# Optimization experiments

Hardware: AMD Instinct MI355X
Metric: run time of the kernel (lower is better)

Reference implementation:

```python
import jax, jax.numpy as jnp
import numpy as np

B, L, R, D = 64, 512, 512, 512
F_CONV, H = 100, 60

def setup_inputs() -> dict:
    key = jax.random.key(0)
    ks = jax.random.split(key, 8)
    l_lengths = jax.random.randint(ks[0], (B,), L // 2, L + 1)
    r_lengths = jax.random.randint(ks[1], (B,), R // 2, R + 1)
    l_vectors = jax.random.normal(ks[2], (L, B, D), jnp.float32)
    r_vectors = jax.random.normal(ks[3], (R, B, D), jnp.float32)
    Wconv = jax.random.normal(ks[4], (F_CONV, D), jnp.float32) / np.sqrt(D).astype(np.float32)
    bconv = jnp.zeros((F_CONV,), jnp.float32)
    Wd = jax.random.normal(ks[5], (H, 2 * F_CONV), jnp.float32) / np.sqrt(2 * F_CONV).astype(np.float32)
    bd = jnp.zeros((H,), jnp.float32)
    return {"l_lengths": l_lengths, "l_vectors": l_vectors, "r_lengths": r_lengths,
            "r_vectors": r_vectors, "Wconv": Wconv, "bconv": bconv, "Wd": Wd, "bd": bd}

def reference(l_lengths, l_vectors, r_lengths, r_vectors, Wconv, bconv, Wd, bd):
    Lm, Bm, Dm = l_vectors.shape
    Rm = r_vectors.shape[0]
    # masks, seq-first [L,B] like pad_sequence output
    l_mask = (jnp.arange(Lm)[:, None] < l_lengths[None, :]).astype(l_vectors.dtype)
    r_mask = (jnp.arange(Rm)[:, None] < r_lengths[None, :]).astype(r_vectors.dtype)
    lmT, rmT = l_mask.T, r_mask.T  # [B,L], [B,R]

    # co-attention scores [B,L,R]
    attention = jnp.einsum('lbd,rbd->blr', l_vectors, r_vectors)
    attention = attention * lmT[:, :, None] * rmT[:, None, :]

    att_r = jax.nn.softmax(attention - 10.0 * (1.0 - lmT[:, :, None]), axis=1)
    att_r = att_r * lmT[:, :, None]
    att_r = att_r / (att_r.sum(axis=1, keepdims=True) + 1e-13)

    att_l = jax.nn.softmax(attention - 10.0 * (1.0 - rmT[:, None, :]), axis=2)
    att_l = att_l * rmT[:, None, :]
    att_l = att_l / (att_l.sum(axis=2, keepdims=True) + 1e-13)

    # ---- left side: stats + top-1 hard attention ----
    rl = r_lengths.astype(l_vectors.dtype)[:, None]
    l_mean = att_l.sum(axis=2) / rl                              # [B,L]
    l_w = (att_l * att_l).sum(axis=2) / rl - l_mean * l_mean
    l_w = l_w / jnp.maximum(l_mean, 0.001)
    l_a = att_l.max(axis=2)                                      # top-1 value [B,L]
    l_i = att_l.argmax(axis=2)                                   # top-1 index [B,L]
    l_i = l_i * lmT.astype(l_i.dtype)
    l_a = l_a / jnp.maximum(l_a, 0.001)                          # k=1: sum == value
    gathered = jnp.take_along_axis(r_vectors, l_i.T[:, :, None], axis=0)  # [L,B,D]
    l_counter = l_a.T[:, :, None] * gathered
    l_c = l_w.T[:, :, None] * jnp.abs(l_vectors - l_counter) * l_mask[:, :, None]

    # ---- right side ----
    ll = l_lengths.astype(r_vectors.dtype)[:, None]
    r_mean = att_r.sum(axis=1) / ll                              # [B,R]
    r_w = (att_r * att_r).sum(axis=1) / ll - r_mean * r_mean
    r_w = r_w / jnp.maximum(r_mean, 0.001)
    r_a = att_r.max(axis=1)                                      # [B,R]
    r_i = att_r.argmax(axis=1)
    r_i = r_i * rmT.astype(r_i.dtype)
    r_a = r_a / jnp.maximum(r_a, 0.001)
    gathered_r = jnp.take_along_axis(l_vectors, r_i.T[:, :, None], axis=0)  # [R,B,D]
    r_counter = r_a.T[:, :, None] * gathered_r
    r_c = r_w.T[:, :, None] * jnp.abs(r_vectors - r_counter) * r_mask[:, :, None]

    # SentenceConv(1, 100, dim): kernel (1, dim) conv == per-position linear,
    # ReLU, masked max-pool over the sequence.
    def sconv(x, mask):  # x [S,B,D], mask [S,B]
        h = jax.nn.relu(jnp.einsum('sbd,fd->bsf', x, Wconv) + bconv)  # [B,S,F]
        h = h - (1.0 - mask.T)[:, :, None] * 1e9
        return h.max(axis=1)  # [B,F]

    feats = jnp.concatenate([sconv(l_c, l_mask), sconv(r_c, r_mask)], axis=1)  # [B,200]
    return jax.nn.relu(feats @ Wd.T + bd)  # [B,60]
```

## Files before the change

kernel.cpp:

```cpp
#include <hip/hip_runtime.h>
#include <math.h>

#define BB 64
#define LL 512
#define RR 512
#define DD 512
#define FC 100
#define FP 112
#define HH 60
#define BD (BB*DD)

typedef __attribute__((ext_vector_type(8))) short bf16x8;
typedef __attribute__((ext_vector_type(4))) float f32x4;

__device__ __forceinline__ unsigned short bf16rne(float x) {
  unsigned u = __float_as_uint(x);
  return (unsigned short)((u + 0x7fffu + ((u >> 16) & 1u)) >> 16);
}
__device__ __forceinline__ float bf16tof(unsigned short h) {
  return __uint_as_float((unsigned)h << 16);
}

__device__ __forceinline__ void split2(float x0, float x1, unsigned& h2, unsigned& l2) {
  unsigned u0 = __float_as_uint(x0), u1 = __float_as_uint(x1);
  h2 = __builtin_amdgcn_perm(u1, u0, 0x07060302u);
  float r0 = x0 - __uint_as_float(u0 & 0xffff0000u);
  float r1 = x1 - __uint_as_float(u1 & 0xffff0000u);
  l2 = __builtin_amdgcn_perm(__float_as_uint(r1), __float_as_uint(r0), 0x07060302u);
}

template <int N>
__device__ __forceinline__ float ror_max_f(float v) {
  return fmaxf(v, __uint_as_float(__builtin_amdgcn_mov_dpp(__float_as_uint(v), 0x120 | N, 0xf, 0xf, true)));
}
template <int N>
__device__ __forceinline__ float ror_add_f(float v) {
  return v + __uint_as_float(__builtin_amdgcn_mov_dpp(__float_as_uint(v), 0x120 | N, 0xf, 0xf, true));
}
template <int N>
__device__ __forceinline__ int ror_min_i(int v) {
  int o = __builtin_amdgcn_mov_dpp(v, 0x120 | N, 0xf, 0xf, true);
  return o < v ? o : v;
}
__device__ __forceinline__ float row16_max(float v) {
  v = ror_max_f<1>(v); v = ror_max_f<2>(v); v = ror_max_f<4>(v); return ror_max_f<8>(v);
}
__device__ __forceinline__ float row16_sum(float v) {
  v = ror_add_f<1>(v); v = ror_add_f<2>(v); v = ror_add_f<4>(v); return ror_add_f<8>(v);
}
__device__ __forceinline__ int row16_min(int v) {
  v = ror_min_i<1>(v); v = ror_min_i<2>(v); v = ror_min_i<4>(v); return ror_min_i<8>(v);
}

__global__ __launch_bounds__(512, 2) void gemm_att(const float* __restrict__ lv,
                                                   const float* __restrict__ rv,
                                                   const int* __restrict__ llen,
                                                   const int* __restrict__ rlen,
                                                   float4* __restrict__ lpart,
                                                   float4* __restrict__ rpart) {
  __shared__ __align__(16) unsigned short Ah[256][40];
  __shared__ __align__(16) unsigned short Al[256][40];
  __shared__ __align__(16) unsigned short Bh[256][40];
  __shared__ __align__(16) unsigned short Bl[256][40];

  const int bid = blockIdx.x;
  const int wid = (bid & 7) * 32 + (bid >> 3);
  const int b  = wid >> 2;
  const int l0 = ((wid >> 1) & 1) * 256;
  const int r0 = (wid & 1) * 256;

  const int t = threadIdx.x;
  const int srow = t >> 1;
  const int half = t & 1;
  const int kq = half * 16;

  const float* Abase = lv + (size_t)(l0 + srow) * BD + b * DD + kq;
  const float* Bbase = rv + (size_t)(r0 + srow) * BD + b * DD + kq;

  float4 pa[4], pb[4];
#pragma unroll
  for (int q = 0; q < 4; ++q) {
    pa[q] = *(const float4*)(Abase + q * 4);
    pb[q] = *(const float4*)(Bbase + q * 4);
  }

  const int lane = t & 63;
  const int wv = t >> 6;
  const int wrow = wv >> 2;
  const int wcol = wv & 3;
  const int fr = lane & 15;
  const int kh = lane >> 4;

  f32x4 acc[8][4];
#pragma unroll
  for (int i = 0; i < 8; ++i)
#pragma unroll
    for (int j = 0; j < 4; ++j) acc[i][j] = (f32x4){0.f, 0.f, 0.f, 0.f};

  for (int it = 0; it < 16; ++it) {
    __syncthreads();
#pragma unroll
    for (int q = 0; q < 4; ++q) {
      unsigned h01, l01, h23, l23;
      split2(pa[q].x, pa[q].y, h01, l01);
      split2(pa[q].z, pa[q].w, h23, l23);
      *(uint2*)&Ah[srow][kq + q * 4] = make_uint2(h01, h23);
      *(uint2*)&Al[srow][kq + q * 4] = make_uint2(l01, l23);
      split2(pb[q].x, pb[q].y, h01, l01);
      split2(pb[q].z, pb[q].w, h23, l23);
      *(uint2*)&Bh[srow][kq + q * 4] = make_uint2(h01, h23);
      *(uint2*)&Bl[srow][kq + q * 4] = make_uint2(l01, l23);
    }
    if (it < 15) {
      const float* An = Abase + (it + 1) * 32;
      const float* Bn = Bbase + (it + 1) * 32;
#pragma unroll
      for (int q = 0; q < 4; ++q) {
        pa[q] = *(const float4*)(An + q * 4);
        pb[q] = *(const float4*)(Bn + q * 4);
      }
    }
    __syncthreads();

    bf16x8 bh[4], bl[4];
#pragma unroll
    for (int j = 0; j < 4; ++j) {
      bh[j] = *(const bf16x8*)&Bh[wcol * 64 + j * 16 + fr][kh * 8];
      bl[j] = *(const bf16x8*)&Bl[wcol * 64 + j * 16 + fr][kh * 8];
    }
#pragma unroll
    for (int i = 0; i < 8; ++i) {
      bf16x8 ah = *(const bf16x8*)&Ah[wrow * 128 + i * 16 + fr][kh * 8];
      bf16x8 al = *(const bf16x8*)&Al[wrow * 128 + i * 16 + fr][kh * 8];
#pragma unroll
      for (int j = 0; j < 4; ++j) {
        acc[i][j] = __builtin_amdgcn_mfma_f32_16x16x32_bf16(ah, bh[j], acc[i][j], 0, 0, 0);
        acc[i][j] = __builtin_amdgcn_mfma_f32_16x16x32_bf16(ah, bl[j], acc[i][j], 0, 0, 0);
        acc[i][j] = __builtin_amdgcn_mfma_f32_16x16x32_bf16(al, bh[j], acc[i][j], 0, 0, 0);
      }
    }
  }

  const int ll_ = llen[b], rl_ = rlen[b];
  __syncthreads();
  float4* rowsc = (float4*)&Ah[0][0];
  float4* colsc = (float4*)&Bh[0][0];

  const int rbase = r0 + wcol * 64 + fr;
  bool vr4[4]; int rr4[4];
#pragma unroll
  for (int j = 0; j < 4; ++j) { rr4[j] = rbase + j * 16; vr4[j] = rr4[j] < rl_; }

#pragma unroll
  for (int i = 0; i < 8; ++i) {
#pragma unroll
    for (int q = 0; q < 4; ++q) {
      const int trow = wrow * 128 + i * 16 + kh * 4 + q;
      const bool vl = (l0 + trow) < ll_;
      float s[4];
      float M = -1e30f;
#pragma unroll
      for (int j = 0; j < 4; ++j) {
        float raw = acc[i][j][q];
        s[j] = !vr4[j] ? -10.f : (vl ? raw : 0.f);
        M = fmaxf(M, s[j]);
      }
      M = row16_max(M);
      float zv = 0.f, q2 = 0.f;
      int loc = 0x7fffffff;
#pragma unroll
      for (int j = 0; j < 4; ++j) {
        float e = __expf(s[j] - M);
        if (vr4[j]) {
          zv += e; q2 += e * e;
          if (s[j] == M && rr4[j] < loc) loc = rr4[j];
        }
      }
      zv = row16_sum(zv);
      q2 = row16_sum(q2);
      loc = row16_min(loc);
      if (fr == 0)
        rowsc[wcol * 256 + trow] = make_float4(M, zv, q2, __int_as_float(loc));
    }
  }

#pragma unroll
  for (int j = 0; j < 4; ++j) {
    const int tcol = wcol * 64 + j * 16 + fr;
    const bool vr = (r0 + tcol) < rl_;
    float M = -1e30f;
#pragma unroll
    for (int i = 0; i < 8; ++i)
#pragma unroll
      for (int q = 0; q < 4; ++q) {
        int lg = l0 + wrow * 128 + i * 16 + kh * 4 + q;
        bool vl = lg < ll_;
        float sv = !vl ? -10.f : (vr ? acc[i][j][q] : 0.f);
        M = fmaxf(M, sv);
      }
    M = fmaxf(M, __shfl_xor(M, 16, 64));
    M = fmaxf(M, __shfl_xor(M, 32, 64));
    float zv = 0.f, q2 = 0.f;
    int loc = 0x7fffffff;
#pragma unroll
    for (int i = 0; i < 8; ++i)
#pragma unroll
      for (int q = 0; q < 4; ++q) {
        int lg = l0 + wrow * 128 + i * 16 + kh * 4 + q;
        bool vl = lg < ll_;
        float sv = !vl ? -10.f : (vr ? acc[i][j][q] : 0.f);
        float e = __expf(sv - M);
        if (vl) {
          zv += e; q2 += e * e;
          if (sv == M && lg < loc) loc = lg;
        }
      }
    zv += __shfl_xor(zv, 16, 64); zv += __shfl_xor(zv, 32, 64);
    q2 += __shfl_xor(q2, 16, 64); q2 += __shfl_xor(q2, 32, 64);
    { int o = __shfl_xor(loc, 16, 64); loc = o < loc ? o : loc; }
    { int o = __shfl_xor(loc, 32, 64); loc = o < loc ? o : loc; }
    if (kh == 0)
      colsc[wrow * 256 + tcol] = make_float4(M, zv, q2, __int_as_float(loc));
  }

  __syncthreads();

  if (t < 256) {
    float4 p = rowsc[t];
    float M = p.x, zv = p.y, q2 = p.z;
    int loc = __float_as_int(p.w);
#pragma unroll
    for (int w2 = 1; w2 < 4; ++w2) {
      float4 o = rowsc[w2 * 256 + t];
      float M1 = o.x;
      float Mn = fmaxf(M, M1);
      float c0 = __expf(M - Mn), c1 = __expf(M1 - Mn);
      zv = zv * c0 + o.y * c1;
      q2 = q2 * c0 * c0 + o.z * c1 * c1;
      int loc1 = __float_as_int(o.w);
      loc = (M1 > M) ? loc1 : ((M1 == M && loc1 < loc) ? loc1 : loc);
      M = Mn;
    }
    lpart[((size_t)(b * 512 + l0 + t)) * 2 + (r0 >> 8)] =
        make_float4(M, zv, q2, __int_as_float(loc));
  } else {
    const int c = t - 256;
    float4 p = colsc[c];
    float M = p.x, zv = p.y, q2 = p.z;
    int loc = __float_as_int(p.w);
    {
      float4 o = colsc[256 + c];
      float M1 = o.x;
      float Mn = fmaxf(M, M1);
      float c0 = __expf(M - Mn), c1 = __expf(M1 - Mn);
      zv = zv * c0 + o.y * c1;
      q2 = q2 * c0 * c0 + o.z * c1 * c1;
      int loc1 = __float_as_int(o.w);
      loc = (M1 > M) ? loc1 : ((M1 == M && loc1 < loc) ? loc1 : loc);
      M = Mn;
    }
    rpart[((size_t)(b * 512 + r0 + c)) * 2 + (l0 >> 8)] =
        make_float4(M, zv, q2, __int_as_float(loc));
  }
}

__global__ __launch_bounds__(256) void stats_merge(const float4* __restrict__ lpart,
    const float4* __restrict__ rpart,
    const int* __restrict__ llen, const int* __restrict__ rlen,
    float* __restrict__ lwv, float* __restrict__ lan, int* __restrict__ lidx,
    float* __restrict__ rwv, float* __restrict__ ran, int* __restrict__ ridx) {
  const int gid = blockIdx.x * 256 + threadIdx.x;
  const int side = gid >> 15;
  const int pos = gid & 32767;
  const int b = pos >> 9, p = pos & 511;
  const float4* part = (side ? rpart : lpart) + (size_t)pos * 2;
  float4 P0 = part[0], P1 = part[1];
  float M = P0.x, zv = P0.y, q2 = P0.z;
  int loc = __float_as_int(P0.w);
  {
    float M1 = P1.x;
    float Mn = fmaxf(M, M1);
    float c0 = __expf(M - Mn), c1 = __expf(M1 - Mn);
    zv = zv * c0 + P1.y * c1;
    q2 = q2 * c0 * c0 + P1.z * c1 * c1;
    int loc1 = __float_as_int(P1.w);
    loc = (M1 > M) ? loc1 : ((M1 == M && loc1 < loc) ? loc1 : loc);
    M = Mn;
  }
  const int len = side ? llen[b] : rlen[b];
  const int own = side ? rlen[b] : llen[b];
  const int ninv = side ? (LL - llen[b]) : (RR - rlen[b]);
  float z0 = zv + (float)ninv * __expf(-10.f - M);
  float S = zv / z0;
  float inv = 1.f / (S + 1e-13f);
  float sumq = S * inv;
  float mean = sumq / (float)len;
  float sumq2 = q2 / (z0 * z0) * inv * inv;
  float var = sumq2 / (float)len - mean * mean;
  float wv = var / fmaxf(mean, 0.001f);
  float qmax = inv / z0;
  float an = qmax / fmaxf(qmax, 0.001f);
  int idx = (p < own && loc != 0x7fffffff) ? loc : 0;
  if (side == 0) { lwv[pos] = wv; lan[pos] = an; lidx[pos] = idx; }
  else           { rwv[pos] = wv; ran[pos] = an; ridx[pos] = idx; }
}

__global__ void prep_w(const float* __restrict__ Wconv,
                       unsigned short* __restrict__ Whg, unsigned short* __restrict__ Wlg) {
  int i = blockIdx.x * 256 + threadIdx.x;
  if (i < FP * DD) {
    int f = i >> 9;
    float w = (f < FC) ? Wconv[i] : 0.f;
    unsigned short h = bf16rne(w);
    unsigned short l = bf16rne(w - bf16tof(h));
    Whg[i] = h; Wlg[i] = l;
  }
}

__global__ __launch_bounds__(256) void conv_pool_mfma(const float* __restrict__ lv,
    const float* __restrict__ rv,
    const float* __restrict__ lwv, const float* __restrict__ lan, const int* __restrict__ lidx,
    const float* __restrict__ rwv, const float* __restrict__ ran, const int* __restrict__ ridx,
    const int* __restrict__ llen, const int* __restrict__ rlen,
    const unsigned short* __restrict__ Whg, const unsigned short* __restrict__ Wlg,
    const float* __restrict__ bconv, float* __restrict__ feat) {
  __shared__ __align__(16) unsigned short Ah[128][40];
  __shared__ __align__(16) unsigned short Al[128][40];
  __shared__ __align__(16) unsigned short Wh[FP][40];
  __shared__ __align__(16) unsigned short Wl[FP][40];
  __shared__ float pool[4][FP];
  __shared__ float ppw[128], ppa[128];
  __shared__ int   ppi[128], ppv[128];

  const int bid = blockIdx.x;
  const int wid = (bid & 7) * 64 + (bid >> 3);
  const int side = wid >> 8;
  const int b    = (wid >> 2) & 63;
  const int s0   = (wid & 3) * 128;

  const int t = threadIdx.x;
  const float* x; const float* y; const float* wb; const float* ab; const int* ib; int plen;
  if (side == 0) { x = lv; y = rv; wb = lwv; ab = lan; ib = lidx; plen = llen[b]; }
  else           { x = rv; y = lv; wb = rwv; ab = ran; ib = ridx; plen = rlen[b]; }

  if (t < 128) {
    int pos = s0 + t;
    ppw[t] = wb[b * 512 + pos];
    ppa[t] = ab[b * 512 + pos];
    ppi[t] = ib[b * 512 + pos];
    ppv[t] = (pos < plen) ? 1 : 0;
  }
  __syncthreads();

  const int pos  = t >> 1;
  const int half = t & 1;
  const float w_ = ppw[pos];
  const float a_ = ppa[pos];
  const int   yi = ppi[pos];
  const float* xp = x + (size_t)(s0 + pos) * BD + b * DD + half * 16;
  const float* yp = y + (size_t)yi * BD + b * DD + half * 16;

  float4 xv[4], yv[4];
#pragma unroll
  for (int q = 0; q < 4; ++q) {
    xv[q] = *(const float4*)(xp + q * 4);
    yv[q] = *(const float4*)(yp + q * 4);
  }

  const int lane = t & 63;
  const int wvi = t >> 6;
  const int m0 = wvi * 32;
  const int fr = lane & 15;
  const int kh = lane >> 4;

  f32x4 acc[2][7];
#pragma unroll
  for (int i = 0; i < 2; ++i)
#pragma unroll
    for (int j = 0; j < 7; ++j) acc[i][j] = (f32x4){0.f, 0.f, 0.f, 0.f};

  for (int it = 0; it < 16; ++it) {
    const int k0 = it * 32;
    __syncthreads();
#pragma unroll
    for (int q = 0; q < 2; ++q) {
      float d0 = w_ * fabsf(xv[2*q].x   - a_ * yv[2*q].x);
      float d1 = w_ * fabsf(xv[2*q].y   - a_ * yv[2*q].y);
      float d2 = w_ * fabsf(xv[2*q].z   - a_ * yv[2*q].z);
      float d3 = w_ * fabsf(xv[2*q].w   - a_ * yv[2*q].w);
      float d4 = w_ * fabsf(xv[2*q+1].x - a_ * yv[2*q+1].x);
      float d5 = w_ * fabsf(xv[2*q+1].y - a_ * yv[2*q+1].y);
      float d6 = w_ * fabsf(xv[2*q+1].z - a_ * yv[2*q+1].z);
      float d7 = w_ * fabsf(xv[2*q+1].w - a_ * yv[2*q+1].w);
      unsigned h01, l01, h23, l23, h45, l45, h67, l67;
      split2(d0, d1, h01, l01);
      split2(d2, d3, h23, l23);
      split2(d4, d5, h45, l45);
      split2(d6, d7, h67, l67);
      *(uint4*)&Ah[pos][half * 16 + q * 8] = make_uint4(h01, h23, h45, h67);
      *(uint4*)&Al[pos][half * 16 + q * 8] = make_uint4(l01, l23, l45, l67);
    }
#pragma unroll
    for (int rep = 0; rep < 2; ++rep) {
      int idx = t + rep * 256;
      if (idx < FP * 4) {
        int f = idx >> 2, q = idx & 3;
        *(ulonglong2*)&Wh[f][q * 8] = *(const ulonglong2*)&Whg[f * DD + k0 + q * 8];
        *(ulonglong2*)&Wl[f][q * 8] = *(const ulonglong2*)&Wlg[f * DD + k0 + q * 8];
      }
    }
    if (it < 15) {
      const float* xn = xp + k0 + 32;
      const float* yn = yp + k0 + 32;
#pragma unroll
      for (int q = 0; q < 4; ++q) {
        xv[q] = *(const float4*)(xn + q * 4);
        yv[q] = *(const float4*)(yn + q * 4);
      }
    }
    __syncthreads();

    bf16x8 ah[2], al[2];
#pragma unroll
    for (int i = 0; i < 2; ++i) {
      ah[i] = *(const bf16x8*)&Ah[m0 + i * 16 + fr][kh * 8];
      al[i] = *(const bf16x8*)&Al[m0 + i * 16 + fr][kh * 8];
    }
#pragma unroll
    for (int j = 0; j < 7; ++j) {
      bf16x8 bh = *(const bf16x8*)&Wh[j * 16 + fr][kh * 8];
      bf16x8 bl = *(const bf16x8*)&Wl[j * 16 + fr][kh * 8];
#pragma unroll
      for (int i = 0; i < 2; ++i) {
        acc[i][j] = __builtin_amdgcn_mfma_f32_16x16x32_bf16(ah[i], bh, acc[i][j], 0, 0, 0);
        acc[i][j] = __builtin_amdgcn_mfma_f32_16x16x32_bf16(ah[i], bl, acc[i][j], 0, 0, 0);
        acc[i][j] = __builtin_amdgcn_mfma_f32_16x16x32_bf16(al[i], bh, acc[i][j], 0, 0, 0);
      }
    }
  }

#pragma unroll
  for (int j = 0; j < 7; ++j) {
    int f = j * 16 + fr;
    float bcv = (f < FC) ? bconv[f] : 0.f;
    float vmax = -1e30f;
#pragma unroll
    for (int i = 0; i < 2; ++i) {
#pragma unroll
      for (int q = 0; q < 4; ++q) {
        int sl = m0 + i * 16 + kh * 4 + q;
        if (ppv[sl]) vmax = fmaxf(vmax, fmaxf(acc[i][j][q] + bcv, 0.f));
      }
    }
    vmax = fmaxf(vmax, __shfl_xor(vmax, 16, 64));
    vmax = fmaxf(vmax, __shfl_xor(vmax, 32, 64));
    if (lane < 16) pool[wvi][f] = vmax;
  }
  __syncthreads();
  if (t < FC) {
    float v = fmaxf(fmaxf(pool[0][t], pool[1][t]), fmaxf(pool[2][t], pool[3][t]));
    if (v > -1e29f) atomicMax((int*)&feat[b * 200 + side * FC + t], __float_as_int(v));
  }
}

__global__ void dense_out(const float* __restrict__ feat, const float* __restrict__ Wd,
                          const float* __restrict__ bd, float* __restrict__ out) {
  int b = blockIdx.x, h = threadIdx.x;
  if (h < HH) {
    float s = bd[h];
    const float* fb = feat + b * 200;
    const float* wr = Wd + h * 200;
    for (int k = 0; k < 200; ++k) s += fb[k] * wr[k];
    out[b * HH + h] = fmaxf(s, 0.f);
  }
}

extern "C" void kernel_launch(void* const* d_in, const int* in_sizes, int n_in,
                              void* d_out, int out_size, void* d_ws, size_t ws_size,
                              hipStream_t stream) {
  (void)in_sizes; (void)n_in; (void)out_size; (void)ws_size;
  const int*   llen  = (const int*)d_in[0];
  const float* lv    = (const float*)d_in[1];
  const int*   rlen  = (const int*)d_in[2];
  const float* rv    = (const float*)d_in[3];
  const float* Wconv = (const float*)d_in[4];
  const float* bconv = (const float*)d_in[5];
  const float* Wd    = (const float*)d_in[6];
  const float* bd    = (const float*)d_in[7];
  float* out = (float*)d_out;
  char* ws = (char*)d_ws;
  size_t off = 0;
  unsigned short* Whg = (unsigned short*)(ws + off); off += (size_t)FP * DD * 2;
  unsigned short* Wlg = (unsigned short*)(ws + off); off += (size_t)FP * DD * 2;
  float4* lpart = (float4*)(ws + off); off += (size_t)BB * LL * 2 * 16;
  float4* rpart = (float4*)(ws + off); off += (size_t)BB * RR * 2 * 16;
  float* lwv = (float*)(ws + off); off += (size_t)BB * LL * 4;
  float* lan = (float*)(ws + off); off += (size_t)BB * LL * 4;
  int*   lidx= (int*)  (ws + off); off += (size_t)BB * LL * 4;
  float* rwv = (float*)(ws + off); off += (size_t)BB * RR * 4;
  float* ran = (float*)(ws + off); off += (size_t)BB * RR * 4;
  int*   ridx= (int*)  (ws + off); off += (size_t)BB * RR * 4;
  float* feat= (float*)(ws + off); off += (size_t)BB * 200 * 4;

  hipMemsetAsync(feat, 0, BB * 200 * 4, stream);
  prep_w<<<(FP * DD + 255) / 256, 256, 0, stream>>>(Wconv, Whg, Wlg);
  gemm_att<<<dim3(256), 512, 0, stream>>>(lv, rv, llen, rlen, lpart, rpart);
  stats_merge<<<dim3(256), 256, 0, stream>>>(lpart, rpart, llen, rlen,
                                             lwv, lan, lidx, rwv, ran, ridx);
  conv_pool_mfma<<<dim3(512), 256, 0, stream>>>(lv, rv, lwv, lan, lidx,
                                                rwv, ran, ridx, llen, rlen,
                                                Whg, Wlg, bconv, feat);
  dense_out<<<BB, 64, 0, stream>>>(feat, Wd, bd, out);
}
```

Measured before the change: 121.0 us.

## Double-buffer LDS tiles and XOR-swizzle layout in attention GEMM

New measurement: 129.0 us. 6.6% more time.

```diff
diff --git a/kernel.cpp b/kernel.cpp
--- a/kernel.cpp
+++ b/kernel.cpp
@@ -29,6 +29,14 @@
   l2 = __builtin_amdgcn_perm(__float_as_uint(r1), __float_as_uint(r0), 0x07060302u);
 }
 
+__device__ __forceinline__ void stage_pair(float4 p0, float4 p1, uint4& hv, uint4& lvv) {
+  unsigned h01, l01, h23, l23, h45, l45, h67, l67;
+  split2(p0.x, p0.y, h01, l01); split2(p0.z, p0.w, h23, l23);
+  split2(p1.x, p1.y, h45, l45); split2(p1.z, p1.w, h67, l67);
+  hv = make_uint4(h01, h23, h45, h67);
+  lvv = make_uint4(l01, l23, l45, l67);
+}
+
 template <int N>
 __device__ __forceinline__ float ror_max_f(float v) {
   return fmaxf(v, __uint_as_float(__builtin_amdgcn_mov_dpp(__float_as_uint(v), 0x120 | N, 0xf, 0xf, true)));
@@ -58,10 +66,10 @@
                                                    const int* __restrict__ rlen,
                                                    float4* __restrict__ lpart,
                                                    float4* __restrict__ rpart) {
-  __shared__ __align__(16) unsigned short Ah[256][40];
-  __shared__ __align__(16) unsigned short Al[256][40];
-  __shared__ __align__(16) unsigned short Bh[256][40];
-  __shared__ __align__(16) unsigned short Bl[256][40];
+  __shared__ __align__(16) unsigned short Ah[2][256][32];
+  __shared__ __align__(16) unsigned short Al[2][256][32];
+  __shared__ __align__(16) unsigned short Bh[2][256][32];
+  __shared__ __align__(16) unsigned short Bl[2][256][32];
 
   const int bid = blockIdx.x;
   const int wid = (bid & 7) * 32 + (bid >> 3);
@@ -72,17 +80,12 @@
   const int t = threadIdx.x;
   const int srow = t >> 1;
   const int half = t & 1;
-  const int kq = half * 16;
-
-  const float* Abase = lv + (size_t)(l0 + srow) * BD + b * DD + kq;
-  const float* Bbase = rv + (size_t)(r0 + srow) * BD + b * DD + kq;
-
-  float4 pa[4], pb[4];
-#pragma unroll
-  for (int q = 0; q < 4; ++q) {
-    pa[q] = *(const float4*)(Abase + q * 4);
-    pb[q] = *(const float4*)(Bbase + q * 4);
-  }
+
+  const float* Abase = lv + (size_t)(l0 + srow) * BD + b * DD + half * 16;
+  const float* Bbase = rv + (size_t)(r0 + srow) * BD + b * DD + half * 16;
+
+  const int sl0 = (((2 * half) ^ ((srow >> 1) & 3)) * 8);
+  const int sl1 = (((2 * half + 1) ^ ((srow >> 1) & 3)) * 8);
 
   const int lane = t & 63;
   const int wv = t >> 6;
@@ -90,6 +93,24 @@
   const int wcol = wv & 3;
   const int fr = lane & 15;
   const int kh = lane >> 4;
+  const int koff = (kh ^ ((fr >> 1) & 3)) * 8;
+
+  float4 pa[4], pb[4];
+#define LOADCHUNK(n) { const float* An = Abase + (n) * 32; const float* Bn = Bbase + (n) * 32; \
+    pa[0] = *(const float4*)(An);     pa[1] = *(const float4*)(An + 4); \
+    pa[2] = *(const float4*)(An + 8); pa[3] = *(const float4*)(An + 12); \
+    pb[0] = *(const float4*)(Bn);     pb[1] = *(const float4*)(Bn + 4); \
+    pb[2] = *(const float4*)(Bn + 8); pb[3] = *(const float4*)(Bn + 12); }
+
+#define STAGE(nb) { uint4 hv, lvv; \
+    stage_pair(pa[0], pa[1], hv, lvv); \
+    *(uint4*)&Ah[nb][srow][sl0] = hv; *(uint4*)&Al[nb][srow][sl0] = lvv; \
+    stage_pair(pa[2], pa[3], hv, lvv); \
+    *(uint4*)&Ah[nb][srow][sl1] = hv; *(uint4*)&Al[nb][srow][sl1] = lvv; \
+    stage_pair(pb[0], pb[1], hv, lvv); \
+    *(uint4*)&Bh[nb][srow][sl0] = hv; *(uint4*)&Bl[nb][srow][sl0] = lvv; \
+    stage_pair(pb[2], pb[3], hv, lvv); \
+    *(uint4*)&Bh[nb][srow][sl1] = hv; *(uint4*)&Bl[nb][srow][sl1] = lvv; }
 
   f32x4 acc[8][4];
 #pragma unroll
@@ -97,54 +118,44 @@
 #pragma unroll
     for (int j = 0; j < 4; ++j) acc[i][j] = (f32x4){0.f, 0.f, 0.f, 0.f};
 
-  for (int it = 0; it < 16; ++it) {
+#define COMPUTE(cb) { bf16x8 bh4[4], bl4[4]; \
+    _Pragma("unroll") \
+    for (int j = 0; j < 4; ++j) { \
+      bh4[j] = *(const bf16x8*)&Bh[cb][wcol * 64 + j * 16 + fr][koff]; \
+      bl4[j] = *(const bf16x8*)&Bl[cb][wcol * 64 + j * 16 + fr][koff]; \
+    } \
+    _Pragma("unroll") \
+    for (int i = 0; i < 8; ++i) { \
+      bf16x8 ah = *(const bf16x8*)&Ah[cb][wrow * 128 + i * 16 + fr][koff]; \
+      bf16x8 al = *(const bf16x8*)&Al[cb][wrow * 128 + i * 16 + fr][koff]; \
+      _Pragma("unroll") \
+      for (int j = 0; j < 4; ++j) { \
+        acc[i][j] = __builtin_amdgcn_mfma_f32_16x16x32_bf16(ah, bh4[j], acc[i][j], 0, 0, 0); \
+        acc[i][j] = __builtin_amdgcn_mfma_f32_16x16x32_bf16(ah, bl4[j], acc[i][j], 0, 0, 0); \
+        acc[i][j] = __builtin_amdgcn_mfma_f32_16x16x32_bf16(al, bh4[j], acc[i][j], 0, 0, 0); \
+      } \
+    } }
+
+  LOADCHUNK(0);
+  STAGE(0);
+  LOADCHUNK(1);
+  __syncthreads();
+
+  for (int it2 = 0; it2 < 8; ++it2) {
+    const int it = it2 * 2;
+    STAGE(1);
+    if (it < 14) LOADCHUNK(it + 2);
+    COMPUTE(0);
     __syncthreads();
-#pragma unroll
-    for (int q = 0; q < 4; ++q) {
-      unsigned h01, l01, h23, l23;
-      split2(pa[q].x, pa[q].y, h01, l01);
-      split2(pa[q].z, pa[q].w, h23, l23);
-      *(uint2*)&Ah[srow][kq + q * 4] = make_uint2(h01, h23);
-      *(uint2*)&Al[srow][kq + q * 4] = make_uint2(l01, l23);
-      split2(pb[q].x, pb[q].y, h01, l01);
-      split2(pb[q].z, pb[q].w, h23, l23);
-      *(uint2*)&Bh[srow][kq + q * 4] = make_uint2(h01, h23);
-      *(uint2*)&Bl[srow][kq + q * 4] = make_uint2(l01, l23);
-    }
-    if (it < 15) {
-      const float* An = Abase + (it + 1) * 32;
-      const float* Bn = Bbase + (it + 1) * 32;
-#pragma unroll
-      for (int q = 0; q < 4; ++q) {
-        pa[q] = *(const float4*)(An + q * 4);
-        pb[q] = *(const float4*)(Bn + q * 4);
-      }
-    }
+    if (it + 1 < 15) STAGE(0);
+    if (it + 1 < 14) LOADCHUNK(it + 3);
+    COMPUTE(1);
     __syncthreads();
-
-    bf16x8 bh[4], bl[4];
-#pragma unroll
-    for (int j = 0; j < 4; ++j) {
-      bh[j] = *(const bf16x8*)&Bh[wcol * 64 + j * 16 + fr][kh * 8];
-      bl[j] = *(const bf16x8*)&Bl[wcol * 64 + j * 16 + fr][kh * 8];
-    }
-#pragma unroll
-    for (int i = 0; i < 8; ++i) {
-      bf16x8 ah = *(const bf16x8*)&Ah[wrow * 128 + i * 16 + fr][kh * 8];
-      bf16x8 al = *(const bf16x8*)&Al[wrow * 128 + i * 16 + fr][kh * 8];
-#pragma unroll
-      for (int j = 0; j < 4; ++j) {
-        acc[i][j] = __builtin_amdgcn_mfma_f32_16x16x32_bf16(ah, bh[j], acc[i][j], 0, 0, 0);
-        acc[i][j] = __builtin_amdgcn_mfma_f32_16x16x32_bf16(ah, bl[j], acc[i][j], 0, 0, 0);
-        acc[i][j] = __builtin_amdgcn_mfma_f32_16x16x32_bf16(al, bh[j], acc[i][j], 0, 0, 0);
-      }
-    }
   }
 
   const int ll_ = llen[b], rl_ = rlen[b];
-  __syncthreads();
-  float4* rowsc = (float4*)&Ah[0][0];
-  float4* colsc = (float4*)&Bh[0][0];
+  float4* rowsc = (float4*)&Ah[0][0][0];
+  float4* colsc = (float4*)&Bh[0][0][0];
 
   const int rbase = r0 + wcol * 64 + fr;
   bool vr4[4]; int rr4[4];
```
